# Kernel tuning notes

Measured on AMD Instinct MI355X. Metric: run time of the kernel, lower is better.

The kernel has to match this reference:

```python
import jax, jax.numpy as jnp
import numpy as np

ALPHA = 0.05      # SSGConv alpha
K_HOPS = 2        # SSGConv K
K_EIG = 16        # Laplacian PE eigenvectors
LN_EPS = 1e-5     # nn.LayerNorm default eps


def setup_inputs() -> dict:
    key = jax.random.key(0)
    ks = jax.random.split(key, 8)
    B, N, T, D = 16, 19, 1024, 64
    return {
        "features": jax.random.normal(ks[0], (B, N, T, D), jnp.float32),
        "adjacency": jax.random.uniform(ks[1], (B, T, N, N), jnp.float32),
        # edge_transform: nn.Linear(1,1)
        "edge_w": jax.random.normal(ks[2], (), jnp.float32) * 0.5,
        "edge_b": jnp.zeros((), jnp.float32),
        # SSGConv internal linear layers (out = h @ W.T + b)
        "gnn0_W": jax.random.normal(ks[3], (D, D + K_EIG), jnp.float32) / jnp.sqrt(jnp.float32(D + K_EIG)),
        "gnn0_b": jnp.zeros((D,), jnp.float32),
        "gnn1_W": jax.random.normal(ks[4], (D, D), jnp.float32) / jnp.sqrt(jnp.float32(D)),
        "gnn1_b": jnp.zeros((D,), jnp.float32),
        "ln0_g": jnp.ones((D,), jnp.float32), "ln0_b": jnp.zeros((D,), jnp.float32),
        "ln1_g": jnp.ones((D,), jnp.float32), "ln1_b": jnp.zeros((D,), jnp.float32),
    }


def _layernorm(x, g, b):
    mu = x.mean(-1, keepdims=True)
    var = ((x - mu) ** 2).mean(-1, keepdims=True)
    return (x - mu) * jax.lax.rsqrt(var + LN_EPS) * g + b


def _gcn_norm_dense(adj, edge_w, edge_b):
    """Edge transform + softplus on existing edges, then PyG gcn_norm.

    adj: (G, N, N). Existing edges are adj>0; their weights are
    softplus(w*a + b). Nodes without a self-loop get one with weight 1
    (add_remaining_self_loops). deg is the scatter over target (column) index.
    """
    G, N, _ = adj.shape
    mask = (adj > 0).astype(adj.dtype)
    w = jax.nn.softplus(adj * edge_w + edge_b) * mask
    eye = jnp.eye(N, dtype=adj.dtype)
    diag_mask = jnp.diagonal(mask, axis1=-2, axis2=-1)  # (G, N)
    w = w + (1.0 - diag_mask)[:, :, None] * eye          # remaining self-loops
    deg = w.sum(axis=-2)                                 # (G, N) column sums (target deg)
    dis = jnp.where(deg > 0, jax.lax.rsqrt(jnp.maximum(deg, 1e-30)), 0.0)
    # norm(i->j) = dis[i] * w[i,j] * dis[j]
    return dis[:, :, None] * w * dis[:, None, :]


def _dynamic_pe(adj):
    """Batched Laplacian eigenvector PE, faithful to _compute_dynamic_pe_vectorized."""
    G, N, _ = adj.shape
    a32 = adj.astype(jnp.float32)
    deg = jnp.maximum(a32.sum(-1), 1e-6)                 # row-sum degrees, clamped
    dis = jax.lax.rsqrt(deg)
    a_norm = dis[:, :, None] * a32 * dis[:, None, :]
    eye = jnp.eye(N, dtype=jnp.float32)
    lap = eye - a_norm + 1e-5 * eye                      # regularized Laplacian
    _, vecs = jnp.linalg.eigh(lap)                       # ascending eigenvalues
    pe = vecs[..., :K_EIG]                               # (G, N, K)
    signs = jnp.sign(pe.sum(-2, keepdims=True))
    signs = jnp.where(signs == 0, 1.0, signs)
    pe = jnp.nan_to_num(pe * signs, nan=0.0, posinf=1.0, neginf=-1.0)
    return pe


def _ssgconv(a_norm, x, W, b):
    """SSGConv: h = alpha*x + sum_{k=1..K} (1-alpha)/K * P^k x; out = h @ W.T + b.
    Propagation: out[j] = sum_i norm(i->j) x[i]  (source->target flow)."""
    h = ALPHA * x
    xk = x
    for _ in range(K_HOPS):
        xk = jnp.einsum('gij,gid->gjd', a_norm, xk)
        h = h + ((1.0 - ALPHA) / K_HOPS) * xk
    return jnp.einsum('gnd,od->gno', h, W) + b


def reference(features, adjacency, edge_w, edge_b,
              gnn0_W, gnn0_b, gnn1_W, gnn1_b,
              ln0_g, ln0_b, ln1_g, ln1_b):
    B, N, T, D = features.shape
    x = features.transpose(0, 2, 1, 3).reshape(B * T, N, D)   # (G, N, D)
    adj = adjacency.reshape(B * T, N, N)
    a_norm = _gcn_norm_dense(adj, edge_w, edge_b)
    pe = _dynamic_pe(adj).astype(features.dtype)
    # layer 0: input = [x, pe], no residual
    h = _ssgconv(a_norm, jnp.concatenate([x, pe], axis=-1), gnn0_W, gnn0_b)
    h = _layernorm(h, ln0_g, ln0_b)                            # dropout is identity (eval)
    # layer 1: input = previous output, residual add
    h = _ssgconv(a_norm, h, gnn1_W, gnn1_b) + h
    h = _layernorm(h, ln1_g, ln1_b)
    return h.reshape(B, T, N, D).transpose(0, 2, 1, 3)         # (B, N, T, D)
```

## Files before the change

kernel.cpp:

```cpp
#include <hip/hip_runtime.h>
#include <math.h>

#define Nn 19
#define Dd 64
#define KE 16
#define DIN 80
#define Tt 1024
#define Bb 16
#define Gg (Bb*Tt)
#define ALPHAc 0.05f
#define HOPW 0.475f
#define LNEPS 1e-5f

#define AN_STRIDE 384
#define PE_STRIDE 304
#define WS_NEED ((size_t)Gg * (AN_STRIDE + PE_STRIDE) * 4)

__device__ __forceinline__ float softplusf(float x){
  return (x > 0.f) ? (x + log1pf(expf(-x))) : log1pf(expf(x));
}

__device__ __forceinline__ float wsum(float v){
  #pragma unroll
  for (int o = 32; o > 0; o >>= 1) v += __shfl_xor(v, o, 64);
  return v;
}

__device__ __forceinline__ float rlanef(float v, int l){
  return __int_as_float(__builtin_amdgcn_readlane(__float_as_int(v), l));
}

__device__ __forceinline__ void wsync(){
  __asm__ volatile("" ::: "memory");
  __builtin_amdgcn_wave_barrier();
  __asm__ volatile("" ::: "memory");
}

#define ARENA_BYTES 4944
__global__ __launch_bounds__(256)
void eig_kernel(const float* __restrict__ adj,
                const float* __restrict__ ew_p, const float* __restrict__ eb_p,
                float* __restrict__ anW, float* __restrict__ peW)
{
  const int wid  = threadIdx.x >> 6;
  const int lane = threadIdx.x & 63;
  const int g    = blockIdx.x * 4 + wid;

  __shared__ __align__(16) char arenaAll[4 * ARENA_BYTES];
  char* arena = arenaAll + wid * ARENA_BYTES;
  float*  Af  = (float*) (arena);
  float*  Vst = (float*) (arena + 1600);
  float*  adjS= (float*) (arena + 1600);
  float*  peB = (float*) (arena + 3200);
  float*  wS  = (float*) (arena + 3200);
  float*  rsS = (float*) (arena + 4704);
  float*  csS = (float*) (arena + 4784);
  float2* cs2 = (float2*)(arena + 4864);

  const float ew = ew_p[0], eb = eb_p[0];

  for (int idx = lane; idx < Nn*Nn; idx += 64)
    adjS[idx] = adj[(size_t)g*(Nn*Nn) + idx];
  wsync();

  for (int idx = lane; idx < Nn*Nn; idx += 64) {
    int i = idx / Nn, j = idx - i*Nn;
    float a = adjS[idx];
    wS[idx] = (a > 0.f) ? softplusf(a*ew + eb) : ((i == j) ? 1.f : 0.f);
  }
  if (lane < Nn) {
    float rs = 0.f;
    for (int j = 0; j < Nn; ++j) rs += adjS[lane*Nn + j];
    rsS[lane] = rsqrtf(fmaxf(rs, 1e-6f));
  }
  wsync();
  if (lane < Nn) {
    float cs = 0.f;
    for (int i = 0; i < Nn; ++i) cs += wS[i*Nn + lane];
    csS[lane] = (cs > 0.f) ? rsqrtf(fmaxf(cs, 1e-30f)) : 0.f;
  }
  wsync();
  for (int idx = lane; idx < Nn*Nn; idx += 64) {
    int i = idx / Nn, j = idx - i*Nn;
    anW[(size_t)g*AN_STRIDE + j*20 + i] = csS[i]*wS[idx]*csS[j];
  }
  for (int idx = lane; idx < Nn*Nn; idx += 64) {
    int i = idx / Nn, j = idx - i*Nn;
    float anij = rsS[i]*adjS[i*Nn + j]*rsS[j];
    float anji = rsS[j]*adjS[j*Nn + i]*rsS[i];
    Af[i*21 + j] = ((i == j) ? (1.f + 1e-5f) : 0.f) - 0.5f*(anij + anji);
  }
  if (lane < Nn) { Af[lane*21 + 19] = 0.f; Af[lane*21 + 20] = 0.f; }
  wsync();

  int li = 0, lj = 0;
  if (lane < 36) {
    int l = lane, row = 0, cnt = 8;
    while (l >= cnt) { l -= cnt; ++row; --cnt; }
    li = row; lj = row + 1 + l;
  } else if (lane < 45) {
    li = lj = lane - 36;
  } else if (lane < 54) {
    li = lane - 45; lj = 0;
  }
  const int la9 = lane % 9;

  float v[Nn];
  #pragma unroll
  for (int c = 0; c < Nn; ++c) v[c] = (lane == c) ? 1.f : 0.f;

  for (int sweep = 0; sweep < 14; ++sweep) {
    if (sweep) {
      float off = 0.f;
      for (int idx = lane; idx < Nn*21; idx += 64) {
        int i2 = idx / 21, j2 = idx - i2*21;
        float vv = Af[idx];
        off += (j2 > i2 && j2 < Nn) ? vv*vv : 0.f;
      }
      off = wsum(off);
      if (off < 5e-10f) break;
    }

    #pragma unroll 1
    for (int r = 0; r < Nn; ++r) {
      int aA = r + 1 + la9;  if (aA >= Nn) aA -= Nn;
      int bA = r + 18 - la9; if (bA >= Nn) bA -= Nn;
      int pA = min(aA, bA), qA = max(aA, bA);
      float apq = Af[pA*21 + qA];
      float app = Af[pA*22], aqq = Af[qA*22];
      bool act = fabsf(apq) > 1e-12f;
      float tau = (aqq - app) * 0.5f * __builtin_amdgcn_rcpf(apq);
      float tt  = __builtin_amdgcn_sqrtf(fmaf(tau, tau, 1.f));
      float tv  = __builtin_amdgcn_rcpf(tau + ((tau >= 0.f) ? tt : -tt));
      float cN  = __builtin_amdgcn_rsqf(fmaf(tv, tv, 1.f));
      float sN  = tv * cN;
      float cc    = act ? cN : 1.f;
      float ss    = act ? sN : 0.f;
      float sSlot = (aA < bA) ? ss : -ss;
      if (lane < 9) cs2[lane] = make_float2(cc, ss);
      int anyact = __any(act && (lane < 9));
      wsync();

      if (anyact) {
        #pragma unroll
        for (int t2 = 0; t2 < 9; ++t2) {
          float ct = rlanef(cc, t2);
          float st = rlanef(sSlot, t2);
          float vp = v[1 + t2], vq = v[18 - t2];
          v[1 + t2]  = fmaf(ct, vp, -st*vq);
          v[18 - t2] = fmaf(st, vp,  ct*vq);
        }
        if (lane < 45) {
          int ai = li + 1 + r;  if (ai >= Nn) ai -= Nn;
          int bi = 18 - li + r; if (bi >= Nn) bi -= Nn;
          int aj = lj + 1 + r;  if (aj >= Nn) aj -= Nn;
          int bj = 18 - lj + r; if (bj >= Nn) bj -= Nn;
          int pi = min(ai, bi), qi = max(ai, bi);
          int pj = min(aj, bj), qj = max(aj, bj);
          float2 csi = cs2[li], csj = cs2[lj];
          int a00 = (pi < pj) ? pi*21 + pj : pj*21 + pi;
          int a01 = (pi < qj) ? pi*21 + qj : qj*21 + pi;
          int a10 = (qi < pj) ? qi*21 + pj : pj*21 + qi;
          int a11 = (qi < qj) ? qi*21 + qj : qj*21 + qi;
          float App = Af[a00], Apq = Af[a01], Aqp = Af[a10], Aqq = Af[a11];
          float B0 = csj.x*App - csj.y*Apq;
          float B1 = csj.y*App + csj.x*Apq;
          float B2 = csj.x*Aqp - csj.y*Aqq;
          float B3 = csj.y*Aqp + csj.x*Aqq;
          Af[a00] = csi.x*B0 - csi.y*B2;
          Af[a01] = csi.x*B1 - csi.y*B3;
          Af[a10] = csi.y*B0 + csi.x*B2;
          Af[a11] = csi.y*B1 + csi.x*B3;
        } else if (lane < 54) {
          int ai = li + 1 + r;  if (ai >= Nn) ai -= Nn;
          int bi = 18 - li + r; if (bi >= Nn) bi -= Nn;
          int p = min(ai, bi), q = max(ai, bi);
          float2 cs = cs2[li];
          int e0 = (r < p) ? r*21 + p : p*21 + r;
          int e1 = (r < q) ? r*21 + q : q*21 + r;
          float ep = Af[e0], eq = Af[e1];
          Af[e0] = cs.x*ep - cs.y*eq;
          Af[e1] = cs.y*ep + cs.x*eq;
        }
        wsync();
      }

      {
        float t0 = v[0];
        #pragma unroll
        for (int c = 0; c < Nn - 1; ++c) v[c] = v[c + 1];
        v[Nn - 1] = t0;
      }
    }
  }

  #pragma unroll
  for (int c = 0; c < Nn; ++c)
    if (lane < Nn) Vst[c*20 + lane] = v[c];
  wsync();

  if (lane < Nn) {
    float lam = Af[lane*22];
    int rk = 0;
    for (int j = 0; j < Nn; ++j) {
      float lj2 = Af[j*22];
      rk += (lj2 < lam) || (lj2 == lam && j < lane);
    }
    if (rk < KE) {
      float sacc = 0.f;
      for (int n = 0; n < Nn; ++n) sacc += Vst[lane*20 + n];
      float sgn = (sacc < 0.f) ? -1.f : 1.f;
      for (int n = 0; n < Nn; ++n) peB[n*KE + rk] = Vst[lane*20 + n]*sgn;
    }
  }
  wsync();
  for (int idx = lane; idx < Nn*KE; idx += 64)
    peW[(size_t)g*PE_STRIDE + idx] = peB[idx];
}

__global__ __launch_bounds__(64)
void gnn_kernel(const float* __restrict__ feat,
                const float* __restrict__ anW, const float* __restrict__ peW,
                const float* __restrict__ W0, const float* __restrict__ b0,
                const float* __restrict__ W1, const float* __restrict__ b1,
                const float* __restrict__ g0, const float* __restrict__ be0,
                const float* __restrict__ g1, const float* __restrict__ be1,
                float* __restrict__ out)
{
  const int g = blockIdx.x, lane = threadIdx.x;
  const int b = g >> 10, t = g & (Tt - 1);

  const float* an = anW + (size_t)g*AN_STRIDE;

  float xa[Nn], xb[Nn];
  const float* fb = feat + (((size_t)b*Nn)*Tt + t)*Dd + lane;
  #pragma unroll
  for (int n = 0; n < Nn; ++n) xa[n] = fb[(size_t)n*Tt*Dd];
  #pragma unroll
  for (int n = 0; n < Nn; ++n)
    xb[n] = (lane < KE) ? peW[(size_t)g*PE_STRIDE + n*KE + lane] : 0.f;

  float x1a[Nn], x1b[Nn];
  for (int j = 0; j < Nn; ++j) {
    float aa = 0.f, ab = 0.f;
    #pragma unroll
    for (int i = 0; i < Nn; ++i) {
      float av = an[j*20 + i];
      aa = fmaf(av, xa[i], aa);
      ab = fmaf(av, xb[i], ab);
    }
    x1a[j] = aa; x1b[j] = ab;
  }
  float h0a[Nn], h0b[Nn];
  #pragma unroll
  for (int n = 0; n < Nn; ++n) {
    h0a[n] = ALPHAc*xa[n] + HOPW*x1a[n];
    h0b[n] = ALPHAc*xb[n] + HOPW*x1b[n];
  }
  for (int j = 0; j < Nn; ++j) {
    float aa = 0.f, ab = 0.f;
    #pragma unroll
    for (int i = 0; i < Nn; ++i) {
      float av = an[j*20 + i];
      aa = fmaf(av, x1a[i], aa);
      ab = fmaf(av, x1b[i], ab);
    }
    h0a[j] += HOPW*aa;
    h0b[j] += HOPW*ab;
  }

  float acc[Nn];
  #pragma unroll
  for (int n = 0; n < Nn; ++n) acc[n] = 0.f;
  {
    const float* w0p = W0 + lane*DIN;
    #pragma unroll
    for (int kb = 0; kb < 64; kb += 16) {
      float w[16];
      #pragma unroll
      for (int q4 = 0; q4 < 4; ++q4)
        *(float4*)&w[4*q4] = *(const float4*)(w0p + kb + 4*q4);
      #pragma unroll
      for (int kk = 0; kk < 16; ++kk) {
        int k = kb + kk;
        #pragma unroll
        for (int n = 0; n < Nn; ++n)
          acc[n] = fmaf(rlanef(h0a[n], k), w[kk], acc[n]);
      }
    }
    float w[16];
    #pragma unroll
    for (int q4 = 0; q4 < 4; ++q4)
      *(float4*)&w[4*q4] = *(const float4*)(w0p + 64 + 4*q4);
    #pragma unroll
    for (int kk = 0; kk < 16; ++kk) {
      #pragma unroll
      for (int n = 0; n < Nn; ++n)
        acc[n] = fmaf(rlanef(h0b[n], kk), w[kk], acc[n]);
    }
  }
  float yv[Nn];
  {
    float bias = b0[lane], gam = g0[lane], bet = be0[lane];
    #pragma unroll
    for (int n = 0; n < Nn; ++n) {
      float v  = acc[n] + bias;
      float mu = wsum(v)*(1.f/64.f);
      float d  = v - mu;
      float var = wsum(d*d)*(1.f/64.f);
      yv[n] = d*rsqrtf(var + LNEPS)*gam + bet;
    }
  }

  float x1c[Nn];
  for (int j = 0; j < Nn; ++j) {
    float aa = 0.f;
    #pragma unroll
    for (int i = 0; i < Nn; ++i)
      aa = fmaf(an[j*20 + i], yv[i], aa);
    x1c[j] = aa;
  }
  float h1[Nn];
  #pragma unroll
  for (int n = 0; n < Nn; ++n) h1[n] = ALPHAc*yv[n] + HOPW*x1c[n];
  for (int j = 0; j < Nn; ++j) {
    float aa = 0.f;
    #pragma unroll
    for (int i = 0; i < Nn; ++i)
      aa = fmaf(an[j*20 + i], x1c[i], aa);
    h1[j] += HOPW*aa;
  }

  float acc1[Nn];
  #pragma unroll
  for (int n = 0; n < Nn; ++n) acc1[n] = 0.f;
  {
    const float* w1p = W1 + lane*Dd;
    #pragma unroll
    for (int kb = 0; kb < 64; kb += 16) {
      float w[16];
      #pragma unroll
      for (int q4 = 0; q4 < 4; ++q4)
        *(float4*)&w[4*q4] = *(const float4*)(w1p + kb + 4*q4);
      #pragma unroll
      for (int kk = 0; kk < 16; ++kk) {
        int k = kb + kk;
        #pragma unroll
        for (int n = 0; n < Nn; ++n)
          acc1[n] = fmaf(rlanef(h1[n], k), w[kk], acc1[n]);
      }
    }
  }
  {
    float bias = b1[lane], gam = g1[lane], bet = be1[lane];
    float* ob = out + (((size_t)b*Nn)*Tt + t)*Dd + lane;
    #pragma unroll
    for (int n = 0; n < Nn; ++n) {
      float v  = acc1[n] + bias + yv[n];
      float mu = wsum(v)*(1.f/64.f);
      float d  = v - mu;
      float var = wsum(d*d)*(1.f/64.f);
      ob[(size_t)n*Tt*Dd] = d*rsqrtf(var + LNEPS)*gam + bet;
    }
  }
}

__global__ __launch_bounds__(64)
void gcm_mono(
  const float* __restrict__ feat,
  const float* __restrict__ adj,
  const float* __restrict__ ew_p, const float* __restrict__ eb_p,
  const float* __restrict__ W0, const float* __restrict__ b0,
  const float* __restrict__ W1, const float* __restrict__ b1,
  const float* __restrict__ g0, const float* __restrict__ be0,
  const float* __restrict__ g1, const float* __restrict__ be1,
  float* __restrict__ out)
{
  const int g    = blockIdx.x;
  const int lane = threadIdx.x;
  const int b    = g >> 10;
  const int t    = g & (Tt - 1);

  __shared__ float  anS[Nn*Nn];
  __shared__ float  peS[Nn*KE];
  __shared__ double evS[Nn];
  __shared__ float  rsS[Nn];
  __shared__ float  csS[Nn];
  __shared__ __align__(16) char arena[6080];
  double* Ad   = (double*)(arena);
  float*  Vf   = (float*)(arena + 3040);
  float*  adjS = (float*)(arena + 4560);
  float*  hb   = (float*)(arena);

  float xr[Nn];
  const float* fb = feat + (((size_t)b*Nn)*Tt + t)*Dd + lane;
  #pragma unroll
  for (int n = 0; n < Nn; ++n) xr[n] = fb[(size_t)n*Tt*Dd];

  const float ew = ew_p[0], eb = eb_p[0];

  for (int idx = lane; idx < Nn*Nn; idx += 64)
    adjS[idx] = adj[(size_t)g*(Nn*Nn) + idx];
  __syncthreads();

  if (lane < Nn) {
    float rs = 0.f;
    for (int j = 0; j < Nn; ++j) rs += adjS[lane*Nn + j];
    rsS[lane] = rsqrtf(fmaxf(rs, 1e-6f));
  }
  for (int idx = lane; idx < Nn*Nn; idx += 64) {
    int i = idx / Nn, j = idx - i*Nn;
    float a = adjS[idx];
    bool m = a > 0.f;
    float wv = m ? softplusf(a*ew + eb) : ((i == j) ? 1.f : 0.f);
    anS[idx] = wv;
  }
  __syncthreads();
  if (lane < Nn) {
    float cs = 0.f;
    for (int i = 0; i < Nn; ++i) cs += anS[i*Nn + lane];
    csS[lane] = (cs > 0.f) ? rsqrtf(fmaxf(cs, 1e-30f)) : 0.f;
  }
  __syncthreads();
  for (int idx = lane; idx < Nn*Nn; idx += 64) {
    int i = idx / Nn, j = idx - i*Nn;
    anS[idx] = csS[i]*anS[idx]*csS[j];
    float anij = rsS[i]*adjS[i*Nn + j]*rsS[j];
    float anji = rsS[j]*adjS[j*Nn + i]*rsS[i];
    double m = ((i == j) ? (1.0 + 1e-5) : 0.0) - 0.5*((double)anij + (double)anji);
    Ad[i*20 + j] = m;
    Vf[i*20 + j] = (i == j) ? 1.f : 0.f;
  }
  __syncthreads();

  for (int sweep = 0; sweep < 30; ++sweep) {
    double off = 0.0;
    for (int idx = lane; idx < Nn*Nn; idx += 64) {
      int i = idx / Nn, j = idx - i*Nn;
      if (i < j) { double v = Ad[i*20 + j]; off += v*v; }
    }
    #pragma unroll
    for (int o = 32; o > 0; o >>= 1) off += __shfl_xor(off, o, 64);
    if (off < 1e-22) break;
    for (int p = 0; p < Nn - 1; ++p) {
      for (int q = p + 1; q < Nn; ++q) {
        double apq = Ad[p*20 + q];
        if (fabs(apq) > 1e-15) {
          double app = Ad[p*20 + p], aqq = Ad[q*20 + q];
          double tau = (aqq - app) / (2.0*apq);
          double tt  = sqrt(1.0 + tau*tau);
          double tv  = (tau >= 0.0) ? 1.0/(tau + tt) : 1.0/(tau - tt);
          double c   = 1.0/sqrt(1.0 + tv*tv);
          double s   = tv*c;
          double akp = 0.0, akq = 0.0; float vkp = 0.f, vkq = 0.f;
          if (lane < Nn) {
            akp = Ad[lane*20 + p]; akq = Ad[lane*20 + q];
            vkp = Vf[lane*20 + p]; vkq = Vf[lane*20 + q];
          }
          __syncthreads();
          if (lane < Nn) {
            double nkp = c*akp - s*akq;
            double nkq = s*akp + c*akq;
            if (lane == p) {
              nkp = c*c*app - 2.0*c*s*apq + s*s*aqq;
              nkq = 0.0;
            } else if (lane == q) {
              nkp = 0.0;
              nkq = s*s*app + 2.0*c*s*apq + c*c*aqq;
            }
            Ad[lane*20 + p] = nkp; Ad[p*20 + lane] = nkp;
            Ad[lane*20 + q] = nkq; Ad[q*20 + lane] = nkq;
            float fc = (float)c, fs = (float)s;
            Vf[lane*20 + p] = fc*vkp - fs*vkq;
            Vf[lane*20 + q] = fs*vkp + fc*vkq;
          }
          __syncthreads();
        }
      }
    }
  }

  if (lane < Nn) evS[lane] = Ad[lane*20 + lane];
  __syncthreads();
  if (lane < Nn) {
    double lam = evS[lane];
    int r = 0;
    for (int j = 0; j < Nn; ++j) {
      double lj = evS[j];
      r += (lj < lam) || (lj == lam && j < lane);
    }
    if (r < KE) {
      float sacc = 0.f;
      for (int n = 0; n < Nn; ++n) sacc += Vf[n*20 + lane];
      float sgn = (sacc < 0.f) ? -1.f : 1.f;
      for (int n = 0; n < Nn; ++n) peS[n*KE + r] = Vf[n*20 + lane]*sgn;
    }
  }
  __syncthreads();

  {
    float x1[Nn], x2[Nn];
    for (int j = 0; j < Nn; ++j) {
      float a2 = 0.f;
      #pragma unroll
      for (int i = 0; i < Nn; ++i) a2 += anS[i*Nn + j]*xr[i];
      x1[j] = a2;
    }
    for (int j = 0; j < Nn; ++j) {
      float a2 = 0.f;
      #pragma unroll
      for (int i = 0; i < Nn; ++i) a2 += anS[i*Nn + j]*x1[i];
      x2[j] = a2;
    }
    #pragma unroll
    for (int n = 0; n < Nn; ++n)
      hb[n*DIN + lane] = ALPHAc*xr[n] + HOPW*(x1[n] + x2[n]);
  }
  if (lane < KE) {
    float xc[Nn], x1[Nn], x2[Nn];
    #pragma unroll
    for (int n = 0; n < Nn; ++n) xc[n] = peS[n*KE + lane];
    for (int j = 0; j < Nn; ++j) {
      float a2 = 0.f;
      #pragma unroll
      for (int i = 0; i < Nn; ++i) a2 += anS[i*Nn + j]*xc[i];
      x1[j] = a2;
    }
    for (int j = 0; j < Nn; ++j) {
      float a2 = 0.f;
      #pragma unroll
      for (int i = 0; i < Nn; ++i) a2 += anS[i*Nn + j]*x1[i];
      x2[j] = a2;
    }
    #pragma unroll
    for (int n = 0; n < Nn; ++n)
      hb[n*DIN + Dd + lane] = ALPHAc*xc[n] + HOPW*(x1[n] + x2[n]);
  }
  __syncthreads();

  float acc[Nn];
  #pragma unroll
  for (int n = 0; n < Nn; ++n) acc[n] = 0.f;
  {
    const float* w0r = W0 + lane*DIN;
    #pragma unroll 8
    for (int k = 0; k < DIN; ++k) {
      float wv = w0r[k];
      #pragma unroll
      for (int n = 0; n < Nn; ++n) acc[n] += hb[n*DIN + k]*wv;
    }
  }
  float yv[Nn];
  {
    float bias = b0[lane], gam = g0[lane], bet = be0[lane];
    #pragma unroll
    for (int n = 0; n < Nn; ++n) {
      float v  = acc[n] + bias;
      float mu = wsum(v)*(1.f/64.f);
      float d  = v - mu;
      float var = wsum(d*d)*(1.f/64.f);
      yv[n] = d*rsqrtf(var + LNEPS)*gam + bet;
    }
  }

  {
    float x1[Nn], x2[Nn];
    for (int j = 0; j < Nn; ++j) {
      float a2 = 0.f;
      #pragma unroll
      for (int i = 0; i < Nn; ++i) a2 += anS[i*Nn + j]*yv[i];
      x1[j] = a2;
    }
    for (int j = 0; j < Nn; ++j) {
      float a2 = 0.f;
      #pragma unroll
      for (int i = 0; i < Nn; ++i) a2 += anS[i*Nn + j]*x1[i];
      x2[j] = a2;
    }
    __syncthreads();
    #pragma unroll
    for (int n = 0; n < Nn; ++n)
      hb[n*Dd + lane] = ALPHAc*yv[n] + HOPW*(x1[n] + x2[n]);
    __syncthreads();
  }

  float acc1[Nn];
  #pragma unroll
  for (int n = 0; n < Nn; ++n) acc1[n] = 0.f;
  {
    const float* w1r = W1 + lane*Dd;
    #pragma unroll 8
    for (int k = 0; k < Dd; ++k) {
      float wv = w1r[k];
      #pragma unroll
      for (int n = 0; n < Nn; ++n) acc1[n] += hb[n*Dd + k]*wv;
    }
  }
  {
    float bias = b1[lane], gam = g1[lane], bet = be1[lane];
    float* ob = out + (((size_t)b*Nn)*Tt + t)*Dd + lane;
    #pragma unroll
    for (int n = 0; n < Nn; ++n) {
      float v  = acc1[n] + bias + yv[n];
      float mu = wsum(v)*(1.f/64.f);
      float d  = v - mu;
      float var = wsum(d*d)*(1.f/64.f);
      ob[(size_t)n*Tt*Dd] = d*rsqrtf(var + LNEPS)*gam + bet;
    }
  }
}

extern "C" void kernel_launch(void* const* d_in, const int* in_sizes, int n_in,
                              void* d_out, int out_size, void* d_ws, size_t ws_size,
                              hipStream_t stream) {
  (void)in_sizes; (void)n_in; (void)out_size;
  const float* feat = (const float*)d_in[0];
  const float* adj  = (const float*)d_in[1];
  const float* ew   = (const float*)d_in[2];
  const float* eb   = (const float*)d_in[3];
  const float* W0   = (const float*)d_in[4];
  const float* b0   = (const float*)d_in[5];
  const float* W1   = (const float*)d_in[6];
  const float* b1   = (const float*)d_in[7];
  const float* g0   = (const float*)d_in[8];
  const float* be0  = (const float*)d_in[9];
  const float* g1   = (const float*)d_in[10];
  const float* be1  = (const float*)d_in[11];
  float* out = (float*)d_out;

  if (ws_size >= WS_NEED) {
    float* anW = (float*)d_ws;
    float* peW = anW + (size_t)Gg*AN_STRIDE;
    hipLaunchKernelGGL(eig_kernel, dim3(Gg/4), dim3(256), 0, stream,
                       adj, ew, eb, anW, peW);
    hipLaunchKernelGGL(gnn_kernel, dim3(Gg), dim3(64), 0, stream,
                       feat, anW, peW, W0, b0, W1, b1, g0, be0, g1, be1, out);
  } else {
    hipLaunchKernelGGL(gcm_mono, dim3(Gg), dim3(64), 0, stream,
                       feat, adj, ew, eb, W0, b0, W1, b1, g0, be0, g1, be1, out);
  }
}
```

Baseline: 882.0 us.

## Move Jacobi eigenvector accumulation to LDS and skip inactive rotations per pair

Eigenvectors are no longer held as a 19-entry register array per lane with readlane broadcasts and a per-step rotation shift. They now live in shared memory, and 45 lanes each update a float4 slice of one rotated column pair. Each lane also checks a ballot mask and skips updates for pairs whose rotation is inactive. The activity tolerance is raised from 1e-12 to 1e-8, which skips more near-converged rotations at a small cost in accuracy. The change aims to cut register pressure and redundant VALU work in the sweep loop, but it adds LDS traffic and bank-conflict risk.

```diff
diff --git a/kernel.cpp b/kernel.cpp
--- a/kernel.cpp
+++ b/kernel.cpp
@@ -11,6 +11,7 @@
 #define ALPHAc 0.05f
 #define HOPW 0.475f
 #define LNEPS 1e-5f
+#define ACT_TOL 1e-8f
 
 #define AN_STRIDE 384
 #define PE_STRIDE 304
@@ -36,7 +37,7 @@
   __asm__ volatile("" ::: "memory");
 }
 
-#define ARENA_BYTES 4944
+#define ARENA_BYTES 4832
 __global__ __launch_bounds__(256)
 void eig_kernel(const float* __restrict__ adj,
                 const float* __restrict__ ew_p, const float* __restrict__ eb_p,
@@ -49,13 +50,13 @@
   __shared__ __align__(16) char arenaAll[4 * ARENA_BYTES];
   char* arena = arenaAll + wid * ARENA_BYTES;
   float*  Af  = (float*) (arena);
-  float*  Vst = (float*) (arena + 1600);
+  float*  Vf  = (float*) (arena + 1600);
   float*  adjS= (float*) (arena + 1600);
-  float*  peB = (float*) (arena + 3200);
-  float*  wS  = (float*) (arena + 3200);
-  float*  rsS = (float*) (arena + 4704);
-  float*  csS = (float*) (arena + 4784);
-  float2* cs2 = (float2*)(arena + 4864);
+  float*  peB = (float*) (arena + 3136);
+  float*  wS  = (float*) (arena + 3136);
+  float*  rsS = (float*) (arena + 4592);
+  float*  csS = (float*) (arena + 4672);
+  float2* cs2 = (float2*)(arena + 4752);
 
   const float ew = ew_p[0], eb = eb_p[0];
 
@@ -91,6 +92,11 @@
     Af[i*21 + j] = ((i == j) ? (1.f + 1e-5f) : 0.f) - 0.5f*(anij + anji);
   }
   if (lane < Nn) { Af[lane*21 + 19] = 0.f; Af[lane*21 + 20] = 0.f; }
+  wsync();
+  for (int idx = lane; idx < Nn*20; idx += 64) {
+    int c = idx / 20, r2 = idx - c*20;
+    Vf[idx] = (r2 == c) ? 1.f : 0.f;
+  }
   wsync();
 
   int li = 0, lj = 0;
@@ -104,10 +110,8 @@
     li = lane - 45; lj = 0;
   }
   const int la9 = lane % 9;
-
-  float v[Nn];
-  #pragma unroll
-  for (int c = 0; c < Nn; ++c) v[c] = (lane == c) ? 1.f : 0.f;
+  const int jv  = la9;
+  const int mrow = (lane / 9) * 4;
 
   for (int sweep = 0; sweep < 14; ++sweep) {
     if (sweep) {
@@ -128,76 +132,74 @@
       int pA = min(aA, bA), qA = max(aA, bA);
       float apq = Af[pA*21 + qA];
       float app = Af[pA*22], aqq = Af[qA*22];
-      bool act = fabsf(apq) > 1e-12f;
+      bool act = fabsf(apq) > ACT_TOL;
       float tau = (aqq - app) * 0.5f * __builtin_amdgcn_rcpf(apq);
       float tt  = __builtin_amdgcn_sqrtf(fmaf(tau, tau, 1.f));
       float tv  = __builtin_amdgcn_rcpf(tau + ((tau >= 0.f) ? tt : -tt));
       float cN  = __builtin_amdgcn_rsqf(fmaf(tv, tv, 1.f));
       float sN  = tv * cN;
-      float cc    = act ? cN : 1.f;
-      float ss    = act ? sN : 0.f;
-      float sSlot = (aA < bA) ? ss : -ss;
+      float cc  = act ? cN : 1.f;
+      float ss  = act ? sN : 0.f;
       if (lane < 9) cs2[lane] = make_float2(cc, ss);
-      int anyact = __any(act && (lane < 9));
+      unsigned mask9 = (unsigned)__ballot(act) & 0x1FFu;
       wsync();
 
-      if (anyact) {
-        #pragma unroll
-        for (int t2 = 0; t2 < 9; ++t2) {
-          float ct = rlanef(cc, t2);
-          float st = rlanef(sSlot, t2);
-          float vp = v[1 + t2], vq = v[18 - t2];
-          v[1 + t2]  = fmaf(ct, vp, -st*vq);
-          v[18 - t2] = fmaf(st, vp,  ct*vq);
-        }
+      if (mask9) {
         if (lane < 45) {
-          int ai = li + 1 + r;  if (ai >= Nn) ai -= Nn;
-          int bi = 18 - li + r; if (bi >= Nn) bi -= Nn;
-          int aj = lj + 1 + r;  if (aj >= Nn) aj -= Nn;
-          int bj = 18 - lj + r; if (bj >= Nn) bj -= Nn;
-          int pi = min(ai, bi), qi = max(ai, bi);
-          int pj = min(aj, bj), qj = max(aj, bj);
-          float2 csi = cs2[li], csj = cs2[lj];
-          int a00 = (pi < pj) ? pi*21 + pj : pj*21 + pi;
-          int a01 = (pi < qj) ? pi*21 + qj : qj*21 + pi;
-          int a10 = (qi < pj) ? qi*21 + pj : pj*21 + qi;
-          int a11 = (qi < qj) ? qi*21 + qj : qj*21 + qi;
-          float App = Af[a00], Apq = Af[a01], Aqp = Af[a10], Aqq = Af[a11];
-          float B0 = csj.x*App - csj.y*Apq;
-          float B1 = csj.y*App + csj.x*Apq;
-          float B2 = csj.x*Aqp - csj.y*Aqq;
-          float B3 = csj.y*Aqp + csj.x*Aqq;
-          Af[a00] = csi.x*B0 - csi.y*B2;
-          Af[a01] = csi.x*B1 - csi.y*B3;
-          Af[a10] = csi.y*B0 + csi.x*B2;
-          Af[a11] = csi.y*B1 + csi.x*B3;
+          if (((mask9 >> li) | (mask9 >> lj)) & 1u) {
+            int ai = li + 1 + r;  if (ai >= Nn) ai -= Nn;
+            int bi = 18 - li + r; if (bi >= Nn) bi -= Nn;
+            int aj = lj + 1 + r;  if (aj >= Nn) aj -= Nn;
+            int bj = 18 - lj + r; if (bj >= Nn) bj -= Nn;
+            int pi = min(ai, bi), qi = max(ai, bi);
+            int pj = min(aj, bj), qj = max(aj, bj);
+            float2 csi = cs2[li], csj = cs2[lj];
+            int a00 = (pi < pj) ? pi*21 + pj : pj*21 + pi;
+            int a01 = (pi < qj) ? pi*21 + qj : qj*21 + pi;
+            int a10 = (qi < pj) ? qi*21 + pj : pj*21 + qi;
+            int a11 = (qi < qj) ? qi*21 + qj : qj*21 + qi;
+            float App = Af[a00], Apq = Af[a01], Aqp = Af[a10], Aqq = Af[a11];
+            float B0 = csj.x*App - csj.y*Apq;
+            float B1 = csj.y*App + csj.x*Apq;
+            float B2 = csj.x*Aqp - csj.y*Aqq;
+            float B3 = csj.y*Aqp + csj.x*Aqq;
+            Af[a00] = csi.x*B0 - csi.y*B2;
+            Af[a01] = csi.x*B1 - csi.y*B3;
+            Af[a10] = csi.y*B0 + csi.x*B2;
+            Af[a11] = csi.y*B1 + csi.x*B3;
+          }
+          if ((mask9 >> jv) & 1u) {
+            int av = jv + 1 + r;  if (av >= Nn) av -= Nn;
+            int bv = 18 - jv + r; if (bv >= Nn) bv -= Nn;
+            int pv = min(av, bv), qv = max(av, bv);
+            float2 cs = cs2[jv];
+            float4 vp = *(const float4*)(Vf + pv*20 + mrow);
+            float4 vq = *(const float4*)(Vf + qv*20 + mrow);
+            float4 np, nq;
+            np.x = cs.x*vp.x - cs.y*vq.x;  nq.x = cs.y*vp.x + cs.x*vq.x;
+            np.y = cs.x*vp.y - cs.y*vq.y;  nq.y = cs.y*vp.y + cs.x*vq.y;
+            np.z = cs.x*vp.z - cs.y*vq.z;  nq.z = cs.y*vp.z + cs.x*vq.z;
+            np.w = cs.x*vp.w - cs.y*vq.w;  nq.w = cs.y*vp.w + cs.x*vq.w;
+            *(float4*)(Vf + pv*20 + mrow) = np;
+            *(float4*)(Vf + qv*20 + mrow) = nq;
+          }
         } else if (lane < 54) {
-          int ai = li + 1 + r;  if (ai >= Nn) ai -= Nn;
-          int bi = 18 - li + r; if (bi >= Nn) bi -= Nn;
-          int p = min(ai, bi), q = max(ai, bi);
-          float2 cs = cs2[li];
-          int e0 = (r < p) ? r*21 + p : p*21 + r;
-          int e1 = (r < q) ? r*21 + q : q*21 + r;
-          float ep = Af[e0], eq = Af[e1];
-          Af[e0] = cs.x*ep - cs.y*eq;
-          Af[e1] = cs.y*ep + cs.x*eq;
+          if ((mask9 >> li) & 1u) {
+            int ai = li + 1 + r;  if (ai >= Nn) ai -= Nn;
+            int bi = 18 - li + r; if (bi >= Nn) bi -= Nn;
+            int p = min(ai, bi), q = max(ai, bi);
+            float2 cs = cs2[li];
+            int e0 = (r < p) ? r*21 + p : p*21 + r;
+            int e1 = (r < q) ? r*21 + q : q*21 + r;
+            float ep = Af[e0], eq = Af[e1];
+            Af[e0] = cs.x*ep - cs.y*eq;
+            Af[e1] = cs.y*ep + cs.x*eq;
+          }
         }
         wsync();
       }
-
-      {
-        float t0 = v[0];
-        #pragma unroll
-        for (int c = 0; c < Nn - 1; ++c) v[c] = v[c + 1];
-        v[Nn - 1] = t0;
-      }
-    }
-  }
-
-  #pragma unroll
-  for (int c = 0; c < Nn; ++c)
-    if (lane < Nn) Vst[c*20 + lane] = v[c];
-  wsync();
+    }
+  }
 
   if (lane < Nn) {
     float lam = Af[lane*22];
@@ -208,9 +210,9 @@
     }
     if (rk < KE) {
       float sacc = 0.f;
-      for (int n = 0; n < Nn; ++n) sacc += Vst[lane*20 + n];
+      for (int n = 0; n < Nn; ++n) sacc += Vf[lane*20 + n];
       float sgn = (sacc < 0.f) ? -1.f : 1.f;
-      for (int n = 0; n < Nn; ++n) peB[n*KE + rk] = Vst[lane*20 + n]*sgn;
+      for (int n = 0; n < Nn; ++n) peB[n*KE + rk] = Vf[lane*20 + n]*sgn;
     }
   }
   wsync();
```

Result: faster. 796.3 us (-9.7%).
